# Optimization experiments

Measured on AMD Instinct MI355X. Metric: run time of the kernel, lower is better.

## Reference

```python
import jax, jax.numpy as jnp
import numpy as np

T, DIM, H = 1024, 2048, 16
QLR, KVLR = 1024, 512
NOPE, ROPE, VD = 128, 64, 128
QKD = NOPE + ROPE          # 192
IH, ID, TOPK = 16, 128, 256
EPS = 1e-6

def rmsnorm(x, w):
    return x * jax.lax.rsqrt(jnp.mean(x * x, axis=-1, keepdims=True) + EPS) * w

def layernorm(x, w, b, eps=1e-5):
    m = jnp.mean(x, axis=-1, keepdims=True)
    v = jnp.mean((x - m) ** 2, axis=-1, keepdims=True)
    return (x - m) * jax.lax.rsqrt(v + eps) * w + b

def apply_rope(x, cos, sin):
    # non-interleaved: first half = real, second half = imag
    d = x.shape[-1] // 2
    while cos.ndim < x.ndim:
        cos, sin = cos[:, None], sin[:, None]
    x1, x2 = x[..., :d], x[..., d:]
    return jnp.concatenate([x1 * cos - x2 * sin, x1 * sin + x2 * cos], axis=-1)

def hadamard(x):
    # unnormalized Walsh-Hadamard on last dim (power of 2)
    n = x.shape[-1]
    shape = x.shape
    y, h = x, 1
    while h < n:
        y = y.reshape(shape[:-1] + (-1, 2 * h))
        a, b = y[..., :h], y[..., h:]
        y = jnp.concatenate([a + b, a - b], axis=-1)
        h *= 2
    return y.reshape(shape)

def rotate_activation(x):
    # half-swap then Hadamard on each half
    d = x.shape[-1] // 2
    x1, x2 = x[..., :d], x[..., d:]
    return jnp.concatenate([hadamard(x2), hadamard(x1)], axis=-1)

def setup_inputs() -> dict:
    key = jax.random.key(0)
    ks = jax.random.split(key, 10)
    s = 0.02
    w = lambda k, shp: jax.random.normal(k, shp, jnp.float32) * s
    pos = jnp.arange(T, dtype=jnp.float32)
    inv = 1.0 / (10000.0 ** (jnp.arange(0, ROPE, 2, dtype=jnp.float32) / ROPE))
    ang = pos[:, None] * inv[None, :]
    return {
        'hidden_states': jax.random.normal(ks[0], (T, DIM), jnp.float32),
        'rope_cos': jnp.cos(ang), 'rope_sin': jnp.sin(ang),
        'wq_a': w(ks[1], (QLR, DIM)),
        'q_norm_w': jnp.ones((QLR,), jnp.float32),
        'wq_b': w(ks[2], (H * QKD, QLR)),
        'wkv_a': w(ks[3], (KVLR + ROPE, DIM)),
        'kv_norm_w': jnp.ones((KVLR,), jnp.float32),
        'wkv_b': w(ks[4], (H * (NOPE + VD), KVLR)),
        'wo': w(ks[5], (DIM, H * VD)),
        'iq_norm_w': jnp.ones((QLR,), jnp.float32),
        'iwq_b': w(ks[6], (IH * ID, QLR)),
        'iwk': w(ks[7], (IH * ID, DIM)),
        'k_norm_w': jnp.ones((ID,), jnp.float32),
        'k_norm_b': jnp.zeros((ID,), jnp.float32),
        'wproj': w(ks[8], (IH, DIM)),
    }

def reference(hidden_states, rope_cos, rope_sin, wq_a, q_norm_w, wq_b,
              wkv_a, kv_norm_w, wkv_b, wo, iq_norm_w, iwq_b, iwk,
              k_norm_w, k_norm_b, wproj):
    x = hidden_states
    t = x.shape[0]
    qr = x @ wq_a.T                                   # [t, QLR]

    # ---- lightning indexer: top-k causal token selection ----
    iq = (rmsnorm(qr, iq_norm_w) @ iwq_b.T).reshape(t, IH, ID)
    iq = jnp.concatenate([apply_rope(iq[..., :ROPE], rope_cos, rope_sin), iq[..., ROPE:]], -1)
    iq = rotate_activation(iq)
    ik = layernorm((x @ iwk.T).reshape(t, IH, ID), k_norm_w, k_norm_b)
    ik = jnp.concatenate([apply_rope(ik[..., :ROPE], rope_cos, rope_sin), ik[..., ROPE:]], -1)
    ik = rotate_activation(ik)
    w = (x @ wproj.T) * (IH ** -0.5) * (ID ** -0.5)   # [t, IH]
    dots = jax.nn.relu(jnp.einsum('thd,shd->ths', iq, ik)) * w[:, :, None]
    score = dots.sum(axis=1)                          # [t, t]
    rows = jnp.arange(t)
    score = jnp.where(rows[None, :] <= rows[:, None], score, -jnp.inf)
    _, topk_idx = jax.lax.top_k(score, TOPK)          # [t, TOPK]
    valid = topk_idx <= rows[:, None]
    safe_idx = jnp.where(valid, topk_idx, 0)

    # ---- MLA latent projections ----
    q = (rmsnorm(qr, q_norm_w) @ wq_b.T).reshape(t, H, QKD)
    q_nope, q_pe = q[..., :NOPE], q[..., NOPE:]
    q_pe = apply_rope(q_pe, rope_cos, rope_sin)
    kv_a = x @ wkv_a.T                                # [t, KVLR+ROPE]
    kv = rmsnorm(kv_a[:, :KVLR], kv_norm_w)
    k_pe = apply_rope(kv_a[:, KVLR:], rope_cos, rope_sin)
    wkv = wkv_b.reshape(H, NOPE + VD, KVLR)
    w_k, w_v = wkv[:, :NOPE, :], wkv[:, NOPE:, :]
    q_nope_proj = jnp.einsum('thd,hdc->thc', q_nope, w_k)
    q_key = jnp.concatenate([q_nope_proj, q_pe], -1)  # [t, H, KVLR+ROPE]
    kv_key = jnp.concatenate([kv, k_pe], -1)          # [t, KVLR+ROPE]

    # ---- sparse attention over selected indices ----
    sel = kv_key[safe_idx]                            # [t, TOPK, KVLR+ROPE]
    scale = QKD ** -0.5
    logits = jnp.einsum('thc,tkc->thk', q_key, sel) * scale
    logits = jnp.where(valid[:, None, :], logits, -jnp.inf)
    attn = jax.nn.softmax(logits, axis=-1)
    out_latent = jnp.einsum('thk,tkc->thc', attn, sel[..., :KVLR])
    out_v = jnp.einsum('thc,hdc->thd', out_latent, w_v)
    return out_v.reshape(t, H * VD) @ wo.T            # [t, DIM]
```

## Files before the change

kernel.cpp:

```cpp
#include <hip/hip_runtime.h>
#include <hip/hip_bf16.h>
#include <math.h>

#define T_     1024
#define DIM_   2048
#define H_     16
#define QLR_   1024
#define KVLR_  512
#define NOPE_  128
#define ROPE_  64
#define VD_    128
#define QKD_   192
#define IH_    16
#define ID_    128
#define TOPK_  256
#define CKV_   576

#define SCALE_W    0.022097086912079608f
#define SCALE_LOG  0.07216878364870323f

typedef short bfrag __attribute__((ext_vector_type(8)));
typedef float ffrag __attribute__((ext_vector_type(4)));

__device__ __forceinline__ unsigned short f2bf(float f) {
    union { __hip_bfloat16 h; unsigned short u; } c; c.h = __float2bfloat16(f); return c.u;
}
__device__ __forceinline__ float bf2f(unsigned short u) {
    union { unsigned short u; __hip_bfloat16 h; } c; c.u = u; return __bfloat162float(c.h);
}

__global__ __launch_bounds__(256) void cast_hl_k(
    const float* __restrict__ in, unsigned short* __restrict__ hi,
    unsigned short* __restrict__ lo, long n)
{
    long base = ((long)blockIdx.x * 256 + threadIdx.x) * 4;
    if (base >= n) return;
    float4 v = *(const float4*)(in + base);
    ushort4 h4;
    h4.x = f2bf(v.x); h4.y = f2bf(v.y); h4.z = f2bf(v.z); h4.w = f2bf(v.w);
    *(ushort4*)(hi + base) = h4;
    if (lo) {
        ushort4 l4;
        l4.x = f2bf(v.x - bf2f(h4.x));
        l4.y = f2bf(v.y - bf2f(h4.y));
        l4.z = f2bf(v.z - bf2f(h4.z));
        l4.w = f2bf(v.w - bf2f(h4.w));
        *(ushort4*)(lo + base) = l4;
    }
}

struct CastSeg { const float* src; unsigned short* hi; unsigned short* lo; };
struct CastDesc { CastSeg seg[6]; int bstart[7]; int nseg; };

__global__ __launch_bounds__(256) void castm_k(CastDesc d)
{
    int b = blockIdx.x, s = 0;
    #pragma unroll
    for (int i = 1; i < 6; ++i) if (i < d.nseg && b >= d.bstart[i]) s = i;
    long base = ((long)(b - d.bstart[s]) * 256 + threadIdx.x) * 4;
    float4 v = *(const float4*)(d.seg[s].src + base);
    ushort4 h4;
    h4.x = f2bf(v.x); h4.y = f2bf(v.y); h4.z = f2bf(v.z); h4.w = f2bf(v.w);
    *(ushort4*)(d.seg[s].hi + base) = h4;
    if (d.seg[s].lo) {
        ushort4 l4;
        l4.x = f2bf(v.x - bf2f(h4.x));
        l4.y = f2bf(v.y - bf2f(h4.y));
        l4.z = f2bf(v.z - bf2f(h4.z));
        l4.w = f2bf(v.w - bf2f(h4.w));
        *(ushort4*)(d.seg[s].lo + base) = l4;
    }
}

__global__ __launch_bounds__(256) void qrnorm_k(const float* __restrict__ qr,
    const float* __restrict__ iqw, const float* __restrict__ qw,
    unsigned short* __restrict__ qriq_hi, unsigned short* __restrict__ qriq_lo,
    unsigned short* __restrict__ qrq_hi)
{
    int t = blockIdx.x, tid = threadIdx.x;
    long base = (long)t * QLR_ + tid * 4;
    float4 v = *(const float4*)(qr + base);
    __shared__ float red[256];
    red[tid] = v.x * v.x + v.y * v.y + v.z * v.z + v.w * v.w;
    __syncthreads();
    for (int off = 128; off; off >>= 1) { if (tid < off) red[tid] += red[tid + off]; __syncthreads(); }
    float r = rsqrtf(red[0] / (float)QLR_ + 1e-6f);
    int col = tid * 4;
    float4 wi = *(const float4*)(iqw + col);
    float4 wq = *(const float4*)(qw + col);
    float s[4] = {v.x, v.y, v.z, v.w};
    float wiv[4] = {wi.x, wi.y, wi.z, wi.w};
    float wqv[4] = {wq.x, wq.y, wq.z, wq.w};
    ushort4 h4, l4, g4;
    unsigned short* hp = (unsigned short*)&h4;
    unsigned short* lp = (unsigned short*)&l4;
    unsigned short* gp = (unsigned short*)&g4;
    #pragma unroll
    for (int i = 0; i < 4; ++i) {
        float ai = s[i] * wiv[i] * r;
        float aq = s[i] * wqv[i] * r;
        hp[i] = f2bf(ai);
        lp[i] = f2bf(ai - bf2f(hp[i]));
        gp[i] = f2bf(aq);
    }
    *(ushort4*)(qriq_hi + base) = h4;
    *(ushort4*)(qriq_lo + base) = l4;
    *(ushort4*)(qrq_hi + base) = g4;
}

__global__ __launch_bounds__(256) void tcast_k(const float* __restrict__ in,
                                               unsigned short* __restrict__ out)
{
    int h = blockIdx.z, c0 = blockIdx.x * 32, d0 = blockIdx.y * 32;
    __shared__ float t[32][33];
    int tx = threadIdx.x & 31, ty = threadIdx.x >> 5;
    #pragma unroll
    for (int i = 0; i < 4; ++i)
        t[ty + i * 8][tx] = in[(long)(h * 256 + d0 + ty + i * 8) * 512 + c0 + tx];
    __syncthreads();
    #pragma unroll
    for (int i = 0; i < 4; ++i)
        out[((long)h * 512 + c0 + ty + i * 8) * 128 + d0 + tx] = f2bf(t[tx][ty + i * 8]);
}

__global__ __launch_bounds__(256) void gemm_bt_mfma_k(
    const unsigned short* __restrict__ A, const unsigned short* __restrict__ B,
    void* __restrict__ Cv, long sA, long sB, long sC,
    int lda, int ldb, int ldc, int N, int K, int obf)
{
    A += (long)blockIdx.z * sA;
    B += (long)blockIdx.z * sB;
    __shared__ unsigned short As[128 * 40];
    __shared__ unsigned short Bs[128 * 40];
    const int tid = threadIdx.x;
    const int bm = blockIdx.y * 128, bn = blockIdx.x * 128;
    const int wave = tid >> 6, lane = tid & 63;
    const int wm = (wave >> 1) * 64, wn = (wave & 1) * 64;
    const int lm = lane & 15, quad = lane >> 4;

    ffrag acc[4][4];
    #pragma unroll
    for (int mi = 0; mi < 4; ++mi)
        #pragma unroll
        for (int ni = 0; ni < 4; ++ni)
            #pragma unroll
            for (int r = 0; r < 4; ++r) acc[mi][ni][r] = 0.f;

    const int srow = tid >> 1, shalf = tid & 1;
    const long aoff = (long)(bm + srow) * lda + shalf * 16;
    int brow = bn + srow; if (brow > N - 1) brow = N - 1;
    const long boff = (long)brow * ldb + shalf * 16;
    unsigned short* la = As + srow * 40 + shalf * 16;
    unsigned short* lb = Bs + srow * 40 + shalf * 16;

    uint4 va0 = *(const uint4*)(A + aoff);
    uint4 va1 = *(const uint4*)(A + aoff + 8);
    uint4 vb0 = *(const uint4*)(B + boff);
    uint4 vb1 = *(const uint4*)(B + boff + 8);

    for (int k0 = 0; k0 < K; k0 += 32) {
        __syncthreads();
        *(uint4*)la = va0; *(uint4*)(la + 8) = va1;
        *(uint4*)lb = vb0; *(uint4*)(lb + 8) = vb1;
        __syncthreads();
        if (k0 + 32 < K) {
            va0 = *(const uint4*)(A + aoff + k0 + 32);
            va1 = *(const uint4*)(A + aoff + k0 + 40);
            vb0 = *(const uint4*)(B + boff + k0 + 32);
            vb1 = *(const uint4*)(B + boff + k0 + 40);
        }
        bfrag af[4], bf[4];
        #pragma unroll
        for (int mi = 0; mi < 4; ++mi)
            af[mi] = *(const bfrag*)(As + (wm + mi * 16 + lm) * 40 + quad * 8);
        #pragma unroll
        for (int ni = 0; ni < 4; ++ni)
            bf[ni] = *(const bfrag*)(Bs + (wn + ni * 16 + lm) * 40 + quad * 8);
        #pragma unroll
        for (int mi = 0; mi < 4; ++mi)
            #pragma unroll
            for (int ni = 0; ni < 4; ++ni)
                acc[mi][ni] = __builtin_amdgcn_mfma_f32_16x16x32_bf16(
                    af[mi], bf[ni], acc[mi][ni], 0, 0, 0);
    }

    #pragma unroll
    for (int mi = 0; mi < 4; ++mi)
        #pragma unroll
        for (int ni = 0; ni < 4; ++ni) {
            int n = bn + wn + ni * 16 + lm;
            if (n < N) {
                int mb = bm + wm + mi * 16 + quad * 4;
                if (obf) {
                    unsigned short* C = (unsigned short*)Cv + (long)blockIdx.z * sC;
                    #pragma unroll
                    for (int r = 0; r < 4; ++r)
                        C[(long)(mb + r) * ldc + n] = f2bf(acc[mi][ni][r]);
                } else {
                    float* C = (float*)Cv + (long)blockIdx.z * sC;
                    #pragma unroll
                    for (int r = 0; r < 4; ++r)
                        C[(long)(mb + r) * ldc + n] = acc[mi][ni][r];
                }
            }
        }
}

__global__ __launch_bounds__(256) void gemm_bt64_k(
    const unsigned short* __restrict__ A, const unsigned short* __restrict__ B,
    void* __restrict__ Cv, long sA, long sB, long sC,
    int lda, int ldb, int ldc, int N, int K, int obf)
{
    A += (long)blockIdx.z * sA;
    B += (long)blockIdx.z * sB;
    __shared__ unsigned short As[64 * 72];
    __shared__ unsigned short Bs[64 * 72];
    const int tid = threadIdx.x;
    const int bm = blockIdx.y * 64, bn = blockIdx.x * 64;
    const int wave = tid >> 6, lane = tid & 63;
    const int wm = (wave >> 1) * 32, wn = (wave & 1) * 32;
    const int lm = lane & 15, quad = lane >> 4;

    ffrag acc[2][2];
    #pragma unroll
    for (int mi = 0; mi < 2; ++mi)
        #pragma unroll
        for (int ni = 0; ni < 2; ++ni)
            #pragma unroll
            for (int r = 0; r < 4; ++r) acc[mi][ni][r] = 0.f;

    const int srow = tid >> 2, schunk = tid & 3;
    const long aoff = (long)(bm + srow) * lda + schunk * 8;
    int brow = bn + srow; if (brow > N - 1) brow = N - 1;
    const long boff = (long)brow * ldb + schunk * 8;
    const int loff = srow * 72 + schunk * 8;

    uint4 va0 = *(const uint4*)(A + aoff);
    uint4 va1 = *(const uint4*)(A + aoff + 32);
    uint4 vb0 = *(const uint4*)(B + boff);
    uint4 vb1 = *(const uint4*)(B + boff + 32);

    for (int k0 = 0; k0 < K; k0 += 64) {
        __syncthreads();
        *(uint4*)(As + loff) = va0; *(uint4*)(As + loff + 32) = va1;
        *(uint4*)(Bs + loff) = vb0; *(uint4*)(Bs + loff + 32) = vb1;
        __syncthreads();
        if (k0 + 64 < K) {
            va0 = *(const uint4*)(A + aoff + k0 + 64);
            va1 = *(const uint4*)(A + aoff + k0 + 96);
            vb0 = *(const uint4*)(B + boff + k0 + 64);
            vb1 = *(const uint4*)(B + boff + k0 + 96);
        }
        bfrag af[2][2], bf[2][2];
        #pragma unroll
        for (int mi = 0; mi < 2; ++mi)
            #pragma unroll
            for (int ks = 0; ks < 2; ++ks)
                af[mi][ks] = *(const bfrag*)(As + (wm + mi * 16 + lm) * 72 + ks * 32 + quad * 8);
        #pragma unroll
        for (int ni = 0; ni < 2; ++ni)
            #pragma unroll
            for (int ks = 0; ks < 2; ++ks)
                bf[ni][ks] = *(const bfrag*)(Bs + (wn + ni * 16 + lm) * 72 + ks * 32 + quad * 8);
        #pragma unroll
        for (int mi = 0; mi < 2; ++mi)
            #pragma unroll
            for (int ni = 0; ni < 2; ++ni) {
                acc[mi][ni] = __builtin_amdgcn_mfma_f32_16x16x32_bf16(af[mi][0], bf[ni][0], acc[mi][ni], 0, 0, 0);
                acc[mi][ni] = __builtin_amdgcn_mfma_f32_16x16x32_bf16(af[mi][1], bf[ni][1], acc[mi][ni], 0, 0, 0);
            }
    }

    #pragma unroll
    for (int mi = 0; mi < 2; ++mi)
        #pragma unroll
        for (int ni = 0; ni < 2; ++ni) {
            int n = bn + wn + ni * 16 + lm;
            if (n < N) {
                int mb = bm + wm + mi * 16 + quad * 4;
                if (obf) {
                    unsigned short* C = (unsigned short*)Cv + (long)blockIdx.z * sC;
                    #pragma unroll
                    for (int r = 0; r < 4; ++r)
                        C[(long)(mb + r) * ldc + n] = f2bf(acc[mi][ni][r]);
                } else {
                    float* C = (float*)Cv + (long)blockIdx.z * sC;
                    #pragma unroll
                    for (int r = 0; r < 4; ++r)
                        C[(long)(mb + r) * ldc + n] = acc[mi][ni][r];
                }
            }
        }
}

__global__ __launch_bounds__(256) void gemm3_bt64_k(
    const unsigned short* __restrict__ Ah, const unsigned short* __restrict__ Al,
    const unsigned short* __restrict__ Bh, const unsigned short* __restrict__ Bl,
    float* __restrict__ C, int lda, int ldb, int ldc, int K)
{
    __shared__ unsigned short Ahs[64 * 72], Als[64 * 72], Bhs[64 * 72], Bls[64 * 72];
    const int tid = threadIdx.x;
    const int bm = blockIdx.y * 64, bn = blockIdx.x * 64;
    const int wave = tid >> 6, lane = tid & 63;
    const int wm = (wave >> 1) * 32, wn = (wave & 1) * 32;
    const int lm = lane & 15, quad = lane >> 4;

    ffrag acc[2][2];
    #pragma unroll
    for (int mi = 0; mi < 2; ++mi)
        #pragma unroll
        for (int ni = 0; ni < 2; ++ni)
            #pragma unroll
            for (int r = 0; r < 4; ++r) acc[mi][ni][r] = 0.f;

    const int srow = tid >> 2, schunk = tid & 3;
    const long aoff = (long)(bm + srow) * lda + schunk * 8;
    const long boff = (long)(bn + srow) * ldb + schunk * 8;
    const int loff = srow * 72 + schunk * 8;

    uint4 vah0 = *(const uint4*)(Ah + aoff);
    uint4 vah1 = *(const uint4*)(Ah + aoff + 32);
    uint4 val0 = *(const uint4*)(Al + aoff);
    uint4 val1 = *(const uint4*)(Al + aoff + 32);
    uint4 vbh0 = *(const uint4*)(Bh + boff);
    uint4 vbh1 = *(const uint4*)(Bh + boff + 32);
    uint4 vbl0 = *(const uint4*)(Bl + boff);
    uint4 vbl1 = *(const uint4*)(Bl + boff + 32);

    for (int k0 = 0; k0 < K; k0 += 64) {
        __syncthreads();
        *(uint4*)(Ahs + loff) = vah0; *(uint4*)(Ahs + loff + 32) = vah1;
        *(uint4*)(Als + loff) = val0; *(uint4*)(Als + loff + 32) = val1;
        *(uint4*)(Bhs + loff) = vbh0; *(uint4*)(Bhs + loff + 32) = vbh1;
        *(uint4*)(Bls + loff) = vbl0; *(uint4*)(Bls + loff + 32) = vbl1;
        __syncthreads();
        if (k0 + 64 < K) {
            vah0 = *(const uint4*)(Ah + aoff + k0 + 64);
            vah1 = *(const uint4*)(Ah + aoff + k0 + 96);
            val0 = *(const uint4*)(Al + aoff + k0 + 64);
            val1 = *(const uint4*)(Al + aoff + k0 + 96);
            vbh0 = *(const uint4*)(Bh + boff + k0 + 64);
            vbh1 = *(const uint4*)(Bh + boff + k0 + 96);
            vbl0 = *(const uint4*)(Bl + boff + k0 + 64);
            vbl1 = *(const uint4*)(Bl + boff + k0 + 96);
        }
        bfrag ah[2][2], al[2][2], bh[2][2], bl[2][2];
        #pragma unroll
        for (int mi = 0; mi < 2; ++mi)
            #pragma unroll
            for (int ks = 0; ks < 2; ++ks) {
                ah[mi][ks] = *(const bfrag*)(Ahs + (wm + mi * 16 + lm) * 72 + ks * 32 + quad * 8);
                al[mi][ks] = *(const bfrag*)(Als + (wm + mi * 16 + lm) * 72 + ks * 32 + quad * 8);
            }
        #pragma unroll
        for (int ni = 0; ni < 2; ++ni)
            #pragma unroll
            for (int ks = 0; ks < 2; ++ks) {
                bh[ni][ks] = *(const bfrag*)(Bhs + (wn + ni * 16 + lm) * 72 + ks * 32 + quad * 8);
                bl[ni][ks] = *(const bfrag*)(Bls + (wn + ni * 16 + lm) * 72 + ks * 32 + quad * 8);
            }
        #pragma unroll
        for (int mi = 0; mi < 2; ++mi)
            #pragma unroll
            for (int ni = 0; ni < 2; ++ni) {
                acc[mi][ni] = __builtin_amdgcn_mfma_f32_16x16x32_bf16(ah[mi][0], bh[ni][0], acc[mi][ni], 0, 0, 0);
                acc[mi][ni] = __builtin_amdgcn_mfma_f32_16x16x32_bf16(ah[mi][0], bl[ni][0], acc[mi][ni], 0, 0, 0);
                acc[mi][ni] = __builtin_amdgcn_mfma_f32_16x16x32_bf16(al[mi][0], bh[ni][0], acc[mi][ni], 0, 0, 0);
                acc[mi][ni] = __builtin_amdgcn_mfma_f32_16x16x32_bf16(ah[mi][1], bh[ni][1], acc[mi][ni], 0, 0, 0);
                acc[mi][ni] = __builtin_amdgcn_mfma_f32_16x16x32_bf16(ah[mi][1], bl[ni][1], acc[mi][ni], 0, 0, 0);
                acc[mi][ni] = __builtin_amdgcn_mfma_f32_16x16x32_bf16(al[mi][1], bh[ni][1], acc[mi][ni], 0, 0, 0);
            }
    }

    #pragma unroll
    for (int mi = 0; mi < 2; ++mi)
        #pragma unroll
        for (int ni = 0; ni < 2; ++ni) {
            int n = bn + wn + ni * 16 + lm;
            int mb = bm + wm + mi * 16 + quad * 4;
            #pragma unroll
            for (int r = 0; r < 4; ++r)
                C[(long)(mb + r) * ldc + n] = acc[mi][ni][r];
        }
}

__global__ __launch_bounds__(256) void wtok_k(const float* __restrict__ x,
    const float* __restrict__ wproj, float* __restrict__ wtok)
{
    int t = blockIdx.x, tid = threadIdx.x;
    __shared__ float xs[DIM_];
    for (int c = tid; c < DIM_; c += 256) xs[c] = x[(long)t * DIM_ + c];
    __syncthreads();
    int wave = tid >> 6, lane = tid & 63;
    #pragma unroll
    for (int i = 0; i < 4; ++i) {
        int h = wave * 4 + i;
        float s = 0.f;
        for (int c = lane; c < DIM_; c += 64) s += xs[c] * wproj[(long)h * DIM_ + c];
        for (int off = 32; off; off >>= 1) s += __shfl_xor(s, off, 64);
        if (lane == 0) wtok[(long)t * IH_ + h] = s * SCALE_W;
    }
}

__global__ __launch_bounds__(256) void transform_iq2_k(const float* __restrict__ iq,
    unsigned short* __restrict__ hi, unsigned short* __restrict__ lo,
    const float* __restrict__ cosb, const float* __restrict__ sinb)
{
    int row = blockIdx.x * 4 + (threadIdx.x >> 6);
    int p = threadIdx.x & 63;
    int t = row >> 4;
    float a = iq[(long)row * 128 + p];
    float b = iq[(long)row * 128 + 64 + p];
    float c = cosb[t * 32 + (p & 31)], sn = sinb[t * 32 + (p & 31)];
    float asw = __shfl_xor(a, 32, 64);
    a = (p < 32) ? (a * c - asw * sn) : (asw * sn + a * c);
    #pragma unroll
    for (int h = 1; h < 64; h <<= 1) {
        float a2 = __shfl_xor(a, h, 64);
        float b2 = __shfl_xor(b, h, 64);
        a = (p & h) ? (a2 - a) : (a + a2);
        b = (p & h) ? (b2 - b) : (b + b2);
    }
    unsigned short hb = f2bf(b), ha = f2bf(a);
    hi[(long)row * 128 + p] = hb;
    hi[(long)row * 128 + 64 + p] = ha;
    lo[(long)row * 128 + p] = f2bf(b - bf2f(hb));
    lo[(long)row * 128 + 64 + p] = f2bf(a - bf2f(ha));
}

__global__ __launch_bounds__(256) void transform_ik2_k(const float* __restrict__ ik,
    unsigned short* __restrict__ hi, unsigned short* __restrict__ lo,
    const float* __restrict__ knw, const float* __restrict__ knb,
    const float* __restrict__ cosb, const float* __restrict__ sinb)
{
    int row = blockIdx.x * 4 + (threadIdx.x >> 6);
    int p = threadIdx.x & 63;
    int t = row >> 4;
    float a = ik[(long)row * 128 + p];
    float b = ik[(long)row * 128 + 64 + p];
    float s = a + b;
    #pragma unroll
    for (int o = 1; o < 64; o <<= 1) s += __shfl_xor(s, o, 64);
    float m = s * (1.f / 128.f);
    float da = a - m, db = b - m;
    float v = da * da + db * db;
    #pragma unroll
    for (int o = 1; o < 64; o <<= 1) v += __shfl_xor(v, o, 64);
    float r = rsqrtf(v * (1.f / 128.f) + 1e-5f);
    a = da * r * knw[p] + knb[p];
    b = db * r * knw[64 + p] + knb[64 + p];
    float c = cosb[t * 32 + (p & 31)], sn = sinb[t * 32 + (p & 31)];
    float asw = __shfl_xor(a, 32, 64);
    a = (p < 32) ? (a * c - asw * sn) : (asw * sn + a * c);
    #pragma unroll
    for (int h = 1; h < 64; h <<= 1) {
        float a2 = __shfl_xor(a, h, 64);
        float b2 = __shfl_xor(b, h, 64);
        a = (p & h) ? (a2 - a) : (a + a2);
        b = (p & h) ? (b2 - b) : (b + b2);
    }
    unsigned short hb = f2bf(b), ha = f2bf(a);
    hi[(long)row * 128 + p] = hb;
    hi[(long)row * 128 + 64 + p] = ha;
    lo[(long)row * 128 + p] = f2bf(b - bf2f(hb));
    lo[(long)row * 128 + 64 + p] = f2bf(a - bf2f(ha));
}

__global__ __launch_bounds__(256) void transform_kv2_k(const float* __restrict__ kva,
    unsigned short* __restrict__ kvb, const float* __restrict__ kvnw,
    const float* __restrict__ cosb, const float* __restrict__ sinb)
{
    int t = blockIdx.x, tid = threadIdx.x;
    const float* a = kva + (long)t * CKV_;
    unsigned short* o = kvb + (long)t * CKV_;
    float v0 = a[tid], v1 = a[tid + 256];
    __shared__ float red[256];
    __shared__ float rsh;
    red[tid] = v0 * v0 + v1 * v1; __syncthreads();
    for (int off = 128; off; off >>= 1) { if (tid < off) red[tid] += red[tid + off]; __syncthreads(); }
    if (tid == 0) rsh = rsqrtf(red[0] / (float)KVLR_ + 1e-6f);
    __syncthreads();
    float rs = rsh;
    o[tid]       = f2bf(v0 * rs * kvnw[tid]);
    o[tid + 256] = f2bf(v1 * rs * kvnw[tid + 256]);
    if (tid < 32) {
        float x1 = a[512 + tid], x2 = a[544 + tid];
        float c = cosb[t * 32 + tid], sn = sinb[t * 32 + tid];
        o[512 + tid] = f2bf(x1 * c - x2 * sn);
        o[544 + tid] = f2bf(x1 * sn + x2 * c);
    }
}

__global__ __launch_bounds__(64) void qpe_k(const float* __restrict__ q,
    unsigned short* __restrict__ qkeyb,
    const float* __restrict__ cosb, const float* __restrict__ sinb)
{
    int row = blockIdx.x * 2 + (threadIdx.x >> 5);
    int i = threadIdx.x & 31;
    int t = row / H_;
    const float* qp = q + (long)row * QKD_ + NOPE_;
    float x1 = qp[i], x2 = qp[i + 32];
    float c = cosb[t * 32 + i], sn = sinb[t * 32 + i];
    unsigned short* o = qkeyb + (long)row * CKV_ + 512;
    o[i]      = f2bf(x1 * c - x2 * sn);
    o[i + 32] = f2bf(x1 * sn + x2 * c);
}

__global__ __launch_bounds__(256) void score3_k(
    const unsigned short* __restrict__ iqh, const unsigned short* __restrict__ iql,
    const unsigned short* __restrict__ ikh, const unsigned short* __restrict__ ikl,
    const float* __restrict__ wtok, float* __restrict__ score)
{
    const int bt = blockIdx.y, bs = blockIdx.x;
    if (bs > bt) return;
    __shared__ unsigned short Ah[64 * 72], Al[64 * 72], Bh[64 * 72], Bl[64 * 72];
    __shared__ float wts[64][16];
    const int tid = threadIdx.x;
    const int wave = tid >> 6, lane = tid & 63;
    const int wm = (wave >> 1) * 32, wn = (wave & 1) * 32;
    const int lm = lane & 15, quad = lane >> 4;
    const int t0 = bt * 64, s0 = bs * 64;
    const int srow = tid >> 2, schunk = tid & 3;
    const int loff = srow * 72 + schunk * 8;

    for (int e = tid; e < 1024; e += 256)
        wts[e >> 4][e & 15] = wtok[(long)(t0 + (e >> 4)) * IH_ + (e & 15)];

    const long abase = (long)(t0 + srow) * 2048 + schunk * 8;
    const long bbase = (long)(s0 + srow) * 2048 + schunk * 8;

    uint4 pah0 = *(const uint4*)(iqh + abase);
    uint4 pah1 = *(const uint4*)(iqh + abase + 32);
    uint4 pal0 = *(const uint4*)(iql + abase);
    uint4 pal1 = *(const uint4*)(iql + abase + 32);
    uint4 pbh0 = *(const uint4*)(ikh + bbase);
    uint4 pbh1 = *(const uint4*)(ikh + bbase + 32);
    uint4 pbl0 = *(const uint4*)(ikl + bbase);
    uint4 pbl1 = *(const uint4*)(ikl + bbase + 32);

    float accf[2][2][4] = {};

    for (int h = 0; h < IH_; ++h) {
        ffrag acch[2][2];
        #pragma unroll
        for (int mi = 0; mi < 2; ++mi)
            #pragma unroll
            for (int ni = 0; ni < 2; ++ni)
                #pragma unroll
                for (int r = 0; r < 4; ++r) acch[mi][ni][r] = 0.f;

        #pragma unroll
        for (int k0 = 0; k0 < ID_; k0 += 64) {
            __syncthreads();
            *(uint4*)(Ah + loff) = pah0; *(uint4*)(Ah + loff + 32) = pah1;
            *(uint4*)(Al + loff) = pal0; *(uint4*)(Al + loff + 32) = pal1;
            *(uint4*)(Bh + loff) = pbh0; *(uint4*)(Bh + loff + 32) = pbh1;
            *(uint4*)(Bl + loff) = pbl0; *(uint4*)(Bl + loff + 32) = pbl1;
            __syncthreads();
            int step = h * 2 + (k0 >> 6) + 1;
            if (step < 32) {
                int off = (step >> 1) * 128 + (step & 1) * 64;
                pah0 = *(const uint4*)(iqh + abase + off);
                pah1 = *(const uint4*)(iqh + abase + off + 32);
                pal0 = *(const uint4*)(iql + abase + off);
                pal1 = *(const uint4*)(iql + abase + off + 32);
                pbh0 = *(const uint4*)(ikh + bbase + off);
                pbh1 = *(const uint4*)(ikh + bbase + off + 32);
                pbl0 = *(const uint4*)(ikl + bbase + off);
                pbl1 = *(const uint4*)(ikl + bbase + off + 32);
            }
            bfrag ahf[2][2], alf[2][2], bhf[2][2], blf[2][2];
            #pragma unroll
            for (int mi = 0; mi < 2; ++mi)
                #pragma unroll
                for (int ks = 0; ks < 2; ++ks) {
                    ahf[mi][ks] = *(const bfrag*)(Ah + (wm + mi * 16 + lm) * 72 + ks * 32 + quad * 8);
                    alf[mi][ks] = *(const bfrag*)(Al + (wm + mi * 16 + lm) * 72 + ks * 32 + quad * 8);
                }
            #pragma unroll
            for (int ni = 0; ni < 2; ++ni)
                #pragma unroll
                for (int ks = 0; ks < 2; ++ks) {
                    bhf[ni][ks] = *(const bfrag*)(Bh + (wn + ni * 16 + lm) * 72 + ks * 32 + quad * 8);
                    blf[ni][ks] = *(const bfrag*)(Bl + (wn + ni * 16 + lm) * 72 + ks * 32 + quad * 8);
                }
            #pragma unroll
            for (int mi = 0; mi < 2; ++mi)
                #pragma unroll
                for (int ni = 0; ni < 2; ++ni) {
                    acch[mi][ni] = __builtin_amdgcn_mfma_f32_16x16x32_bf16(ahf[mi][0], bhf[ni][0], acch[mi][ni], 0, 0, 0);
                    acch[mi][ni] = __builtin_amdgcn_mfma_f32_16x16x32_bf16(ahf[mi][0], blf[ni][0], acch[mi][ni], 0, 0, 0);
                    acch[mi][ni] = __builtin_amdgcn_mfma_f32_16x16x32_bf16(alf[mi][0], bhf[ni][0], acch[mi][ni], 0, 0, 0);
                    acch[mi][ni] = __builtin_amdgcn_mfma_f32_16x16x32_bf16(ahf[mi][1], bhf[ni][1], acch[mi][ni], 0, 0, 0);
                    acch[mi][ni] = __builtin_amdgcn_mfma_f32_16x16x32_bf16(ahf[mi][1], blf[ni][1], acch[mi][ni], 0, 0, 0);
                    acch[mi][ni] = __builtin_amdgcn_mfma_f32_16x16x32_bf16(alf[mi][1], bhf[ni][1], acch[mi][ni], 0, 0, 0);
                }
        }
        #pragma unroll
        for (int mi = 0; mi < 2; ++mi) {
            float wr[4];
            #pragma unroll
            for (int r = 0; r < 4; ++r) wr[r] = wts[wm + mi * 16 + quad * 4 + r][h];
            #pragma unroll
            for (int ni = 0; ni < 2; ++ni)
                #pragma unroll
                for (int r = 0; r < 4; ++r)
                    accf[mi][ni][r] += fmaxf(acch[mi][ni][r], 0.f) * wr[r];
        }
    }
    #pragma unroll
    for (int mi = 0; mi < 2; ++mi)
        #pragma unroll
        for (int ni = 0; ni < 2; ++ni) {
            int s = s0 + wn + ni * 16 + lm;
            int tb = t0 + wm + mi * 16 + quad * 4;
            #pragma unroll
            for (int r = 0; r < 4; ++r)
                score[(long)(tb + r) * T_ + s] = accf[mi][ni][r];
        }
}

__global__ __launch_bounds__(512) void topk_k(const float* __restrict__ score, int* __restrict__ topk)
{
    int t = blockIdx.x, tid = threadIdx.x;
    __shared__ float v[1024];
    __shared__ int ix[1024];
    for (int i = tid; i < 1024; i += 512) {
        v[i] = (i <= t) ? score[(long)t * T_ + i] : -INFINITY;
        ix[i] = i;
    }
    __syncthreads();
    for (int k = 2; k <= 1024; k <<= 1) {
        for (int j = k >> 1; j > 0; j >>= 1) {
            for (int i = tid; i < 1024; i += 512) {
                int l = i ^ j;
                if (l > i) {
                    bool up = ((i & k) == 0);
                    float vi = v[i], vl = v[l];
                    int xi = ix[i], xl = ix[l];
                    bool iBetter = (vi > vl) || (vi == vl && xi < xl);
                    bool doSwap = up ? !iBetter : iBetter;
                    if (doSwap) { v[i] = vl; v[l] = vi; ix[i] = xl; ix[l] = xi; }
                }
            }
            __syncthreads();
        }
    }
    if (tid < 256) topk[(long)t * TOPK_ + tid] = ix[tid];
}

__global__ __launch_bounds__(256, 4) void attn3_k(
    const unsigned short* __restrict__ qkeyb, const unsigned short* __restrict__ kvb,
    const int* __restrict__ topkp, unsigned short* __restrict__ olat)
{
    __shared__ __align__(16) unsigned short U[13568];
    __shared__ float red[16 * 17];
    __shared__ int kidx[256];
    unsigned short* Qbf = U;
    float*          Lg  = (float*)U;
    unsigned short* VT0 = U;
    unsigned short* VT1 = U + 4608;
    unsigned short* Pbf = U + 9344;

    const int t = blockIdx.x, tid = threadIdx.x;
    const int wave = tid >> 6, lane = tid & 63;
    const int lm = lane & 15, quad = lane >> 4;

    kidx[tid] = topkp[(long)t * TOPK_ + tid];
    const uint2* q2 = (const uint2*)(qkeyb + (long)t * (H_ * CKV_));
    #pragma unroll
    for (int rep = 0; rep < 9; ++rep) {
        int e = rep * 256 + tid;
        uint2 v = q2[e];
        int f = e * 4, h = f / CKV_, c = f - h * CKV_;
        *(uint2*)(Qbf + h * 584 + c) = v;
    }
    int myk0 = topkp[(long)t * TOPK_ + wave * 64 + 0 * 16 + lm];
    int myk1 = topkp[(long)t * TOPK_ + wave * 64 + 1 * 16 + lm];
    int myk2 = topkp[(long)t * TOPK_ + wave * 64 + 2 * 16 + lm];
    int myk3 = topkp[(long)t * TOPK_ + wave * 64 + 3 * 16 + lm];
    __syncthreads();

    ffrag acc[4];
    #pragma unroll
    for (int ni = 0; ni < 4; ++ni)
        #pragma unroll
        for (int r = 0; r < 4; ++r) acc[ni][r] = 0.f;

    const unsigned short* kb0 = kvb + (long)myk0 * CKV_ + quad * 8;
    const unsigned short* kb1 = kvb + (long)myk1 * CKV_ + quad * 8;
    const unsigned short* kb2 = kvb + (long)myk2 * CKV_ + quad * 8;
    const unsigned short* kb3 = kvb + (long)myk3 * CKV_ + quad * 8;

    bfrag ba[4], bb[4], bc[4];
    #define LDT(DST, C) { \
        DST[0] = *(const bfrag*)(kb0 + (C)); \
        DST[1] = *(const bfrag*)(kb1 + (C)); \
        DST[2] = *(const bfrag*)(kb2 + (C)); \
        DST[3] = *(const bfrag*)(kb3 + (C)); }
    #define PHA_STEP(I, BUF) { \
        bfrag af = *(const bfrag*)(Qbf + lm * 584 + (I) * 32 + quad * 8); \
        _Pragma("unroll") \
        for (int ni = 0; ni < 4; ++ni) \
            acc[ni] = __builtin_amdgcn_mfma_f32_16x16x32_bf16(af, BUF[ni], acc[ni], 0, 0, 0); \
        if ((I) < 15) LDT(BUF, (I) * 32 + 96) }

    LDT(ba, 0) LDT(bb, 32) LDT(bc, 64)
    PHA_STEP(0, ba)  PHA_STEP(1, bb)  PHA_STEP(2, bc)
    PHA_STEP(3, ba)  PHA_STEP(4, bb)  PHA_STEP(5, bc)
    PHA_STEP(6, ba)  PHA_STEP(7, bb)  PHA_STEP(8, bc)
    PHA_STEP(9, ba)  PHA_STEP(10, bb) PHA_STEP(11, bc)
    PHA_STEP(12, ba) PHA_STEP(13, bb) PHA_STEP(14, bc)
    PHA_STEP(15, ba) PHA_STEP(16, bb) PHA_STEP(17, bc)
    #undef PHA_STEP
    #undef LDT

    __syncthreads();
    #pragma unroll
    for (int ni = 0; ni < 4; ++ni)
        #pragma unroll
        for (int r = 0; r < 4; ++r)
            Lg[(quad * 4 + r) * 260 + wave * 64 + ni * 16 + lm] = acc[ni][r];
    __syncthreads();

    {
        int h = tid >> 4, j = tid & 15;
        float m = -INFINITY;
        #pragma unroll
        for (int kk = 0; kk < 16; ++kk) {
            int key = j * 16 + kk;
            if (kidx[key] <= t) m = fmaxf(m, Lg[h * 260 + key]);
        }
        red[h * 17 + j] = m;
        __syncthreads();
        float mh = -INFINITY;
        #pragma unroll
        for (int jj = 0; jj < 16; ++jj) mh = fmaxf(mh, red[h * 17 + jj]);
        __syncthreads();
        float s = 0.f;
        float pv[16];
        #pragma unroll
        for (int kk = 0; kk < 16; ++kk) {
            int key = j * 16 + kk;
            float e = (kidx[key] <= t) ? expf(Lg[h * 260 + key] * SCALE_LOG - mh * SCALE_LOG) : 0.f;
            pv[kk] = e; s += e;
        }
        red[h * 17 + j] = s;
        __syncthreads();
        float sh = 0.f;
        #pragma unroll
        for (int jj = 0; jj < 16; ++jj) sh += red[h * 17 + jj];
        float inv = 1.f / sh;
        #pragma unroll
        for (int kk = 0; kk < 16; ++kk)
            Pbf[h * 264 + j * 16 + kk] = f2bf(pv[kk] * inv);
    }

    const int kpair = tid & 15, cgrp = tid >> 4;
    ffrag acc2[2];
    #pragma unroll
    for (int ci = 0; ci < 2; ++ci)
        #pragma unroll
        for (int r = 0; r < 4; ++r) acc2[ci][r] = 0.f;

    uint4 ga0, gb0, ga1, gb1;
    #define PREFB(GA, GB, IT) { \
        int ka_ = kidx[((IT) & 7) * 32 + 2 * kpair]; \
        int kb_ = kidx[((IT) & 7) * 32 + 2 * kpair + 1]; \
        long co_ = (long)(((IT) >> 3) * 128 + cgrp * 8); \
        GA = *(const uint4*)(kvb + (long)ka_ * CKV_ + co_); \
        GB = *(const uint4*)(kvb + (long)kb_ * CKV_ + co_); }
    #define STOREB(GA, GB, BUF) { \
        const unsigned short* pa_ = (const unsigned short*)&GA; \
        const unsigned short* pb_ = (const unsigned short*)&GB; \
        _Pragma("unroll") \
        for (int i_ = 0; i_ < 8; ++i_) \
            *(unsigned int*)((BUF) + (cgrp * 8 + i_) * 36 + 2 * kpair) = \
                (unsigned int)pa_[i_] | ((unsigned int)pb_[i_] << 16); }
    #define MFMAB(BUF, IT) { \
        bfrag pa = *(const bfrag*)(Pbf + lm * 264 + ((IT) & 7) * 32 + quad * 8); \
        _Pragma("unroll") \
        for (int ci = 0; ci < 2; ++ci) { \
            int c = wave * 32 + ci * 16 + lm; \
            bfrag bv; \
            ((uint2*)&bv)[0] = *(const uint2*)((BUF) + c * 36 + quad * 8); \
            ((uint2*)&bv)[1] = *(const uint2*)((BUF) + c * 36 + quad * 8 + 4); \
            acc2[ci] = __builtin_amdgcn_mfma_f32_16x16x32_bf16(pa, bv, acc2[ci], 0, 0, 0); } }
    #define OLATST(IT) { \
        int p_ = (IT) >> 3; \
        _Pragma("unroll") \
        for (int ci = 0; ci < 2; ++ci) \
            _Pragma("unroll") \
            for (int r = 0; r < 4; ++r) \
                olat[((long)t * H_ + quad * 4 + r) * 512 + p_ * 128 + wave * 32 + ci * 16 + lm] \
                    = f2bf(acc2[ci][r]); \
        _Pragma("unroll") \
        for (int ci = 0; ci < 2; ++ci) \
            _Pragma("unroll") \
            for (int r = 0; r < 4; ++r) acc2[ci][r] = 0.f; }
    #define LGKBAR() { asm volatile("s_waitcnt lgkmcnt(0)" ::: "memory"); \
                       __builtin_amdgcn_s_barrier(); }

    PREFB(ga0, gb0, 0);
    PREFB(ga1, gb1, 1);
    LGKBAR();
    STOREB(ga0, gb0, VT0);
    LGKBAR();
    for (int it = 0; it < 32; it += 2) {
        STOREB(ga1, gb1, VT1);
        MFMAB(VT0, it);
        if (it + 2 < 32) PREFB(ga0, gb0, it + 2);
        LGKBAR();
        if (it + 2 < 32) STOREB(ga0, gb0, VT0);
        MFMAB(VT1, it + 1);
        if (it + 3 < 32) PREFB(ga1, gb1, it + 3);
        if (((it + 1) & 7) == 7) OLATST(it + 1);
        LGKBAR();
    }
    #undef PREFB
    #undef STOREB
    #undef MFMAB
    #undef OLATST
    #undef LGKBAR
}

extern "C" void kernel_launch(void* const* d_in, const int* in_sizes, int n_in,
                              void* d_out, int out_size, void* d_ws, size_t ws_size,
                              hipStream_t stream)
{
    const float* x          = (const float*)d_in[0];
    const float* cosb       = (const float*)d_in[1];
    const float* sinb       = (const float*)d_in[2];
    const float* wq_a       = (const float*)d_in[3];
    const float* q_norm_w   = (const float*)d_in[4];
    const float* wq_b       = (const float*)d_in[5];
    const float* wkv_a      = (const float*)d_in[6];
    const float* kv_norm_w  = (const float*)d_in[7];
    const float* wkv_b      = (const float*)d_in[8];
    const float* wo         = (const float*)d_in[9];
    const float* iq_norm_w  = (const float*)d_in[10];
    const float* iwq_b      = (const float*)d_in[11];
    const float* iwk        = (const float*)d_in[12];
    const float* k_norm_w   = (const float*)d_in[13];
    const float* k_norm_b   = (const float*)d_in[14];
    const float* wproj      = (const float*)d_in[15];
    float* out = (float*)d_out;

    float* ws    = (float*)d_ws;
    float* qr    = ws;
    float* wtok  = ws + 1049600;
    int*   topk  = (int*)(ws + 1655808);
    float* qkey  = ws + 1917952;
    float* outv  = ws + 11355136;
    float* U0    = ws + 13452288;
    float* iq    = U0;
    float* ik    = U0 + 2097152;
    float* kva   = U0 + 4194304;
    float* qbuf  = U0 + 4784128;
    float* score = U0 + 7929856;

    unsigned short* qkey_u = (unsigned short*)qkey;
    unsigned short* wqa_hi  = qkey_u;
    unsigned short* wqa_lo  = qkey_u + 2097152;
    unsigned short* iwk_hi  = qkey_u + 4194304;
    unsigned short* iwk_lo  = qkey_u + 8388608;
    unsigned short* iwqb_hi = qkey_u + 12582912;
    unsigned short* iwqb_lo = qkey_u + 14680064;
    unsigned short* qriq_hi = qkey_u + 16777216;
    unsigned short* qriq_lo = qkey_u + 17825792;
    unsigned short* iqbf_hi = qkey_u;
    unsigned short* iqbf_lo = qkey_u + 2097152;
    unsigned short* ikbf_hi = qkey_u + 4194304;
    unsigned short* ikbf_lo = qkey_u + 6291456;
    unsigned short* qkey_bf = qkey_u;
    unsigned short* wkvb_bf = qkey_u + 9437184;
    unsigned short* wo_bf   = qkey_u + 11534336;
    unsigned short* q_u     = (unsigned short*)qbuf;
    unsigned short* x_hi    = q_u;
    unsigned short* x_lo    = q_u + 2097152;
    unsigned short* wkva_hi = q_u + 4194304;
    unsigned short* outv_u  = (unsigned short*)outv;
    unsigned short* wqb_hi  = outv_u;
    unsigned short* qrq_hi  = outv_u + 3145728;
    unsigned short* outv_bf = outv_u;
    unsigned short* qbf     = (unsigned short*)iq;
    unsigned short* wkT     = (unsigned short*)ik;
    unsigned short* kvb     = (unsigned short*)qr;
    unsigned short* olat_bf = (unsigned short*)U0;

    {
        CastDesc d;
        d.seg[0] = { x,      x_hi,    x_lo    };
        d.seg[1] = { wq_a,   wqa_hi,  wqa_lo  };
        d.seg[2] = { iwk,    iwk_hi,  iwk_lo  };
        d.seg[3] = { iwq_b,  iwqb_hi, iwqb_lo };
        d.seg[4] = { wkv_a,  wkva_hi, nullptr };
        d.seg[5] = { wq_b,   wqb_hi,  nullptr };
        d.bstart[0] = 0;     d.bstart[1] = 2048;  d.bstart[2] = 4096;
        d.bstart[3] = 8192;  d.bstart[4] = 10240; d.bstart[5] = 11392;
        d.bstart[6] = 14464; d.nseg = 6;
        castm_k<<<14464, 256, 0, stream>>>(d);
    }

    gemm3_bt64_k<<<dim3(QLR_/64, T_/64), 256, 0, stream>>>(
        x_hi, x_lo, wqa_hi, wqa_lo, qr, DIM_, DIM_, QLR_, DIM_);

    qrnorm_k<<<T_, 256, 0, stream>>>(qr, iq_norm_w, q_norm_w, qriq_hi, qriq_lo, qrq_hi);

    gemm3_bt64_k<<<dim3(IH_*ID_/64, T_/64), 256, 0, stream>>>(
        qriq_hi, qriq_lo, iwqb_hi, iwqb_lo, iq, QLR_, QLR_, IH_*ID_, QLR_);
    gemm3_bt64_k<<<dim3(IH_*ID_/64, T_/64), 256, 0, stream>>>(
        x_hi, x_lo, iwk_hi, iwk_lo, ik, DIM_, DIM_, IH_*ID_, DIM_);

    gemm_bt64_k<<<dim3((CKV_+63)/64, T_/64, 1), 256, 0, stream>>>(
        x_hi, wkva_hi, kva, 0,0,0, DIM_, DIM_, CKV_, CKV_, DIM_, 0);

    gemm_bt64_k<<<dim3(H_*QKD_/64, T_/64, 1), 256, 0, stream>>>(
        qrq_hi, wqb_hi, qbuf, 0,0,0, QLR_, QLR_, H_*QKD_, H_*QKD_, QLR_, 0);

    wtok_k<<<T_, 256, 0, stream>>>(x, wproj, wtok);

    transform_iq2_k<<<T_*IH_/4, 256, 0, stream>>>(iq, iqbf_hi, iqbf_lo, cosb, sinb);
    transform_ik2_k<<<T_*IH_/4, 256, 0, stream>>>(ik, ikbf_hi, ikbf_lo, k_norm_w, k_norm_b, cosb, sinb);
    transform_kv2_k<<<T_, 256, 0, stream>>>(kva, kvb, kv_norm_w, cosb, sinb);

    score3_k<<<dim3(T_/64, T_/64), 256, 0, stream>>>(iqbf_hi, iqbf_lo, ikbf_hi, ikbf_lo, wtok, score);
    topk_k<<<T_, 512, 0, stream>>>(score, topk);

    cast_hl_k<<<3072, 256, 0, stream>>>(qbuf, qbf, nullptr, 3145728L);
    tcast_k<<<dim3(16, 4, 16), 256, 0, stream>>>(wkv_b, wkT);
    qpe_k<<<T_*H_/2, 64, 0, stream>>>(qbuf, qkey_bf, cosb, sinb);
    gemm_bt_mfma_k<<<dim3(KVLR_/128, T_/128, H_), 256, 0, stream>>>(
        qbf, wkT, qkey_bf, 192L, 65536L, 576L, H_*QKD_, ID_, H_*CKV_, KVLR_, ID_, 1);

    attn3_k<<<T_, 256, 0, stream>>>(qkey_bf, kvb, topk, olat_bf);

    {
        CastDesc d;
        d.seg[0] = { wkv_b, wkvb_bf, nullptr };
        d.seg[1] = { wo,    wo_bf,   nullptr };
        d.seg[2] = d.seg[0]; d.seg[3] = d.seg[0]; d.seg[4] = d.seg[0]; d.seg[5] = d.seg[0];
        d.bstart[0] = 0; d.bstart[1] = 2048; d.bstart[2] = 6144;
        d.bstart[3] = 6144; d.bstart[4] = 6144; d.bstart[5] = 6144; d.bstart[6] = 6144;
        d.nseg = 2;
        castm_k<<<6144, 256, 0, stream>>>(d);
    }

    gemm_bt64_k<<<dim3(VD_/64, T_/64, H_), 256, 0, stream>>>(
        olat_bf, wkvb_bf + (long)NOPE_*KVLR_, outv_bf,
        512L, (long)(NOPE_+VD_)*KVLR_, (long)VD_,
        H_*KVLR_, KVLR_, H_*VD_, VD_, KVLR_, 1);

    gemm_bt64_k<<<dim3(DIM_/64, T_/64, 1), 256, 0, stream>>>(
        outv_bf, wo_bf, out, 0,0,0, H_*VD_, H_*VD_, DIM_, DIM_, H_*VD_, 0);

    (void)in_sizes; (void)n_in; (void)out_size; (void)ws_size;
}
```

Baseline: 535.9 us.

## Merge independent GEMMs, casts and transforms into multi-segment kernel launches

Introduces a generic descriptor-driven kernel that dispatches each block to a GEMM (single or three-pass split bf16), a cast, a transpose-cast, the wtok projection or q rope, based on segment ranges. Independent work such as the q_a and index-k projections plus wtok, or the index-q GEMM with the kv_a GEMM and weight casts, now shares one launch. The per-row transforms are merged into one kernel as well. This cuts launch count and tail idle time, at the cost of a larger shared-memory footprint and more registers in the single-pass GEMM path, plus runtime mode branching.

```diff
diff --git a/kernel.cpp b/kernel.cpp
--- a/kernel.cpp
+++ b/kernel.cpp
@@ -27,26 +27,6 @@
 }
 __device__ __forceinline__ float bf2f(unsigned short u) {
     union { unsigned short u; __hip_bfloat16 h; } c; c.u = u; return __bfloat162float(c.h);
-}
-
-__global__ __launch_bounds__(256) void cast_hl_k(
-    const float* __restrict__ in, unsigned short* __restrict__ hi,
-    unsigned short* __restrict__ lo, long n)
-{
-    long base = ((long)blockIdx.x * 256 + threadIdx.x) * 4;
-    if (base >= n) return;
-    float4 v = *(const float4*)(in + base);
-    ushort4 h4;
-    h4.x = f2bf(v.x); h4.y = f2bf(v.y); h4.z = f2bf(v.z); h4.w = f2bf(v.w);
-    *(ushort4*)(hi + base) = h4;
-    if (lo) {
-        ushort4 l4;
-        l4.x = f2bf(v.x - bf2f(h4.x));
-        l4.y = f2bf(v.y - bf2f(h4.y));
-        l4.z = f2bf(v.z - bf2f(h4.z));
-        l4.w = f2bf(v.w - bf2f(h4.w));
-        *(ushort4*)(lo + base) = l4;
-    }
 }
 
 struct CastSeg { const float* src; unsigned short* hi; unsigned short* lo; };
@@ -108,21 +88,6 @@
     *(ushort4*)(qrq_hi + base) = g4;
 }
 
-__global__ __launch_bounds__(256) void tcast_k(const float* __restrict__ in,
-                                               unsigned short* __restrict__ out)
-{
-    int h = blockIdx.z, c0 = blockIdx.x * 32, d0 = blockIdx.y * 32;
-    __shared__ float t[32][33];
-    int tx = threadIdx.x & 31, ty = threadIdx.x >> 5;
-    #pragma unroll
-    for (int i = 0; i < 4; ++i)
-        t[ty + i * 8][tx] = in[(long)(h * 256 + d0 + ty + i * 8) * 512 + c0 + tx];
-    __syncthreads();
-    #pragma unroll
-    for (int i = 0; i < 4; ++i)
-        out[((long)h * 512 + c0 + ty + i * 8) * 128 + d0 + tx] = f2bf(t[tx][ty + i * 8]);
-}
-
 __global__ __launch_bounds__(256) void gemm_bt_mfma_k(
     const unsigned short* __restrict__ A, const unsigned short* __restrict__ B,
     void* __restrict__ Cv, long sA, long sB, long sC,
@@ -206,17 +171,106 @@
         }
 }
 
-__global__ __launch_bounds__(256) void gemm_bt64_k(
-    const unsigned short* __restrict__ A, const unsigned short* __restrict__ B,
-    void* __restrict__ Cv, long sA, long sB, long sC,
-    int lda, int ldb, int ldc, int N, int K, int obf)
+struct GSeg {
+    const void* A; const void* Al; const void* B; const void* Bl;
+    void* C; void* C2;
+    long sA, sB, sC;
+    int lda, ldb, ldc, N, K, bnx, bmx, mode, obf;
+};
+struct GDesc { GSeg seg[4]; int bstart[5]; int nseg; };
+
+__global__ __launch_bounds__(256) void mgemm_k(GDesc d)
 {
-    A += (long)blockIdx.z * sA;
-    B += (long)blockIdx.z * sB;
-    __shared__ unsigned short As[64 * 72];
-    __shared__ unsigned short Bs[64 * 72];
+    __shared__ unsigned short Ahs[64 * 72], Als[64 * 72], Bhs[64 * 72], Bls[64 * 72];
     const int tid = threadIdx.x;
-    const int bm = blockIdx.y * 64, bn = blockIdx.x * 64;
+    const int b = blockIdx.x;
+    int s = 0;
+    #pragma unroll
+    for (int i = 1; i < 4; ++i) if (i < d.nseg && b >= d.bstart[i]) s = i;
+    const int rel = b - d.bstart[s];
+    const int mode = d.seg[s].mode;
+
+    if (mode == 2) {
+        const float* src = (const float*)d.seg[s].A;
+        unsigned short* hi = (unsigned short*)d.seg[s].C;
+        unsigned short* lo = (unsigned short*)d.seg[s].C2;
+        long base = ((long)rel * 256 + tid) * 4;
+        float4 v = *(const float4*)(src + base);
+        ushort4 h4;
+        h4.x = f2bf(v.x); h4.y = f2bf(v.y); h4.z = f2bf(v.z); h4.w = f2bf(v.w);
+        *(ushort4*)(hi + base) = h4;
+        if (lo) {
+            ushort4 l4;
+            l4.x = f2bf(v.x - bf2f(h4.x));
+            l4.y = f2bf(v.y - bf2f(h4.y));
+            l4.z = f2bf(v.z - bf2f(h4.z));
+            l4.w = f2bf(v.w - bf2f(h4.w));
+            *(ushort4*)(lo + base) = l4;
+        }
+        return;
+    }
+    if (mode == 3) {
+        const float* x = (const float*)d.seg[s].A;
+        const float* wproj = (const float*)d.seg[s].B;
+        float* wt = (float*)d.seg[s].C;
+        float* xs = (float*)Ahs;
+        int t = rel;
+        for (int c = tid; c < DIM_; c += 256) xs[c] = x[(long)t * DIM_ + c];
+        __syncthreads();
+        int wave = tid >> 6, lane = tid & 63;
+        #pragma unroll
+        for (int i = 0; i < 4; ++i) {
+            int h = wave * 4 + i;
+            float sum = 0.f;
+            for (int c = lane; c < DIM_; c += 64) sum += xs[c] * wproj[(long)h * DIM_ + c];
+            for (int off = 32; off; off >>= 1) sum += __shfl_xor(sum, off, 64);
+            if (lane == 0) wt[(long)t * IH_ + h] = sum * SCALE_W;
+        }
+        return;
+    }
+    if (mode == 4) {
+        const float* in = (const float*)d.seg[s].A;
+        unsigned short* out = (unsigned short*)d.seg[s].C;
+        int h = rel >> 6, c0 = (rel & 15) * 32, d0 = ((rel >> 4) & 3) * 32;
+        float (*tt)[33] = (float(*)[33])(void*)Ahs;
+        int tx = tid & 31, ty = tid >> 5;
+        #pragma unroll
+        for (int i = 0; i < 4; ++i)
+            tt[ty + i * 8][tx] = in[(long)(h * 256 + d0 + ty + i * 8) * 512 + c0 + tx];
+        __syncthreads();
+        #pragma unroll
+        for (int i = 0; i < 4; ++i)
+            out[((long)h * 512 + c0 + ty + i * 8) * 128 + d0 + tx] = f2bf(tt[tx][ty + i * 8]);
+        return;
+    }
+    if (mode == 5) {
+        const float* q = (const float*)d.seg[s].A;
+        const float* cosb = (const float*)d.seg[s].B;
+        const float* sinb = (const float*)d.seg[s].Bl;
+        unsigned short* qk = (unsigned short*)d.seg[s].C;
+        int row = rel * 8 + (tid >> 5);
+        int i = tid & 31;
+        int t = row / H_;
+        const float* qp = q + (long)row * QKD_ + NOPE_;
+        float x1 = qp[i], x2 = qp[i + 32];
+        float c = cosb[t * 32 + i], sn = sinb[t * 32 + i];
+        unsigned short* o = qk + (long)row * CKV_ + 512;
+        o[i]      = f2bf(x1 * c - x2 * sn);
+        o[i + 32] = f2bf(x1 * sn + x2 * c);
+        return;
+    }
+
+    const GSeg g = d.seg[s];
+    const bool three = (mode == 1);
+    const int per = g.bnx * g.bmx;
+    const int z = rel / per;
+    const int r2 = rel - z * per;
+    const int bm = (r2 / g.bnx) * 64, bn = (r2 % g.bnx) * 64;
+    const unsigned short* A  = (const unsigned short*)g.A + (long)z * g.sA;
+    const unsigned short* B  = (const unsigned short*)g.B + (long)z * g.sB;
+    const unsigned short* Alp = (const unsigned short*)g.Al;
+    const unsigned short* Blp = (const unsigned short*)g.Bl;
+
     const int wave = tid >> 6, lane = tid & 63;
     const int wm = (wave >> 1) * 32, wn = (wave & 1) * 32;
     const int lm = lane & 15, quad = lane >> 4;
@@ -230,44 +284,81 @@
             for (int r = 0; r < 4; ++r) acc[mi][ni][r] = 0.f;
 
     const int srow = tid >> 2, schunk = tid & 3;
-    const long aoff = (long)(bm + srow) * lda + schunk * 8;
-    int brow = bn + srow; if (brow > N - 1) brow = N - 1;
-    const long boff = (long)brow * ldb + schunk * 8;
+    const long aoff = (long)(bm + srow) * g.lda + schunk * 8;
+    int brow = bn + srow; if (brow > g.N - 1) brow = g.N - 1;
+    const long boff = (long)brow * g.ldb + schunk * 8;
     const int loff = srow * 72 + schunk * 8;
 
-    uint4 va0 = *(const uint4*)(A + aoff);
-    uint4 va1 = *(const uint4*)(A + aoff + 32);
-    uint4 vb0 = *(const uint4*)(B + boff);
-    uint4 vb1 = *(const uint4*)(B + boff + 32);
-
-    for (int k0 = 0; k0 < K; k0 += 64) {
+    uint4 va0, va1, vb0, vb1, wa0, wa1, wb0, wb1;
+    va0 = *(const uint4*)(A + aoff);
+    va1 = *(const uint4*)(A + aoff + 32);
+    vb0 = *(const uint4*)(B + boff);
+    vb1 = *(const uint4*)(B + boff + 32);
+    if (three) {
+        wa0 = *(const uint4*)(Alp + aoff);
+        wa1 = *(const uint4*)(Alp + aoff + 32);
+        wb0 = *(const uint4*)(Blp + boff);
+        wb1 = *(const uint4*)(Blp + boff + 32);
+    }
+
+    for (int k0 = 0; k0 < g.K; k0 += 64) {
         __syncthreads();
-        *(uint4*)(As + loff) = va0; *(uint4*)(As + loff + 32) = va1;
-        *(uint4*)(Bs + loff) = vb0; *(uint4*)(Bs + loff + 32) = vb1;
+        *(uint4*)(Ahs + loff) = va0; *(uint4*)(Ahs + loff + 32) = va1;
+        *(uint4*)(Bhs + loff) = vb0; *(uint4*)(Bhs + loff + 32) = vb1;
+        if (three) {
+            *(uint4*)(Als + loff) = wa0; *(uint4*)(Als + loff + 32) = wa1;
+            *(uint4*)(Bls + loff) = wb0; *(uint4*)(Bls + loff + 32) = wb1;
+        }
         __syncthreads();
-        if (k0 + 64 < K) {
+        if (k0 + 64 < g.K) {
             va0 = *(const uint4*)(A + aoff + k0 + 64);
             va1 = *(const uint4*)(A + aoff + k0 + 96);
             vb0 = *(const uint4*)(B + boff + k0 + 64);
             vb1 = *(const uint4*)(B + boff + k0 + 96);
-        }
-        bfrag af[2][2], bf[2][2];
+            if (three) {
+                wa0 = *(const uint4*)(Alp + aoff + k0 + 64);
+                wa1 = *(const uint4*)(Alp + aoff + k0 + 96);
+                wb0 = *(const uint4*)(Blp + boff + k0 + 64);
+                wb1 = *(const uint4*)(Blp + boff + k0 + 96);
+            }
+        }
+        bfrag ah[2][2], bh[2][2], al[2][2], bl[2][2];
         #pragma unroll
         for (int mi = 0; mi < 2; ++mi)
             #pragma unroll
             for (int ks = 0; ks < 2; ++ks)
-                af[mi][ks] = *(const bfrag*)(As + (wm + mi * 16 + lm) * 72 + ks * 32 + quad * 8);
+                ah[mi][ks] = *(const bfrag*)(Ahs + (wm + mi * 16 + lm) * 72 + ks * 32 + quad * 8);
         #pragma unroll
         for (int ni = 0; ni < 2; ++ni)
             #pragma unroll
             for (int ks = 0; ks < 2; ++ks)
-                bf[ni][ks] = *(const bfrag*)(Bs + (wn + ni * 16 + lm) * 72 + ks * 32 + quad * 8);
+                bh[ni][ks] = *(const bfrag*)(Bhs + (wn + ni * 16 + lm) * 72 + ks * 32 + quad * 8);
+        if (three) {
+            #pragma unroll
+            for (int mi = 0; mi < 2; ++mi)
+                #pragma unroll
+                for (int ks = 0; ks < 2; ++ks)
+                    al[mi][ks] = *(const bfrag*)(Als + (wm + mi * 16 + lm) * 72 + ks * 32 + quad * 8);
+            #pragma unroll
+            for (int ni = 0; ni < 2; ++ni)
+                #pragma unroll
+                for (int ks = 0; ks < 2; ++ks)
+                    bl[ni][ks] = *(const bfrag*)(Bls + (wn + ni * 16 + lm) * 72 + ks * 32 + quad * 8);
+        }
         #pragma unroll
         for (int mi = 0; mi < 2; ++mi)
             #pragma unroll
             for (int ni = 0; ni < 2; ++ni) {
-                acc[mi][ni] = __builtin_amdgcn_mfma_f32_16x16x32_bf16(af[mi][0], bf[ni][0], acc[mi][ni], 0, 0, 0);
-                acc[mi][ni] = __builtin_amdgcn_mfma_f32_16x16x32_bf16(af[mi][1], bf[ni][1], acc[mi][ni], 0, 0, 0);
+                acc[mi][ni] = __builtin_amdgcn_mfma_f32_16x16x32_bf16(ah[mi][0], bh[ni][0], acc[mi][ni], 0, 0, 0);
+                if (three) {
+                    acc[mi][ni] = __builtin_amdgcn_mfma_f32_16x16x32_bf16(ah[mi][0], bl[ni][0], acc[mi][ni], 0, 0, 0);
+                    acc[mi][ni] = __builtin_amdgcn_mfma_f32_16x16x32_bf16(al[mi][0], bh[ni][0], acc[mi][ni], 0, 0, 0);
+                }
+                acc[mi][ni] = __builtin_amdgcn_mfma_f32_16x16x32_bf16(ah[mi][1], bh[ni][1], acc[mi][ni], 0, 0, 0);
+                if (three) {
+                    acc[mi][ni] = __builtin_amdgcn_mfma_f32_16x16x32_bf16(ah[mi][1], bl[ni][1], acc[mi][ni], 0, 0, 0);
+                    acc[mi][ni] = __builtin_amdgcn_mfma_f32_16x16x32_bf16(al[mi][1], bh[ni][1], acc[mi][ni], 0, 0, 0);
+                }
             }
     }
 
@@ -276,234 +367,91 @@
         #pragma unroll
         for (int ni = 0; ni < 2; ++ni) {
             int n = bn + wn + ni * 16 + lm;
-            if (n < N) {
+            if (n < g.N) {
                 int mb = bm + wm + mi * 16 + quad * 4;
-                if (obf) {
-                    unsigned short* C = (unsigned short*)Cv + (long)blockIdx.z * sC;
+                if (g.obf) {
+                    unsigned short* C = (unsigned short*)g.C + (long)z * g.sC;
                     #pragma unroll
                     for (int r = 0; r < 4; ++r)
-                        C[(long)(mb + r) * ldc + n] = f2bf(acc[mi][ni][r]);
+                        C[(long)(mb + r) * g.ldc + n] = f2bf(acc[mi][ni][r]);
                 } else {
-                    float* C = (float*)Cv + (long)blockIdx.z * sC;
+                    float* C = (float*)g.C + (long)z * g.sC;
                     #pragma unroll
                     for (int r = 0; r < 4; ++r)
-                        C[(long)(mb + r) * ldc + n] = acc[mi][ni][r];
+                        C[(long)(mb + r) * g.ldc + n] = acc[mi][ni][r];
                 }
             }
         }
 }
 
-__global__ __launch_bounds__(256) void gemm3_bt64_k(
-    const unsigned short* __restrict__ Ah, const unsigned short* __restrict__ Al,
-    const unsigned short* __restrict__ Bh, const unsigned short* __restrict__ Bl,
-    float* __restrict__ C, int lda, int ldb, int ldc, int K)
-{
-    __shared__ unsigned short Ahs[64 * 72], Als[64 * 72], Bhs[64 * 72], Bls[64 * 72];
-    const int tid = threadIdx.x;
-    const int bm = blockIdx.y * 64, bn = blockIdx.x * 64;
-    const int wave = tid >> 6, lane = tid & 63;
-    const int wm = (wave >> 1) * 32, wn = (wave & 1) * 32;
-    const int lm = lane & 15, quad = lane >> 4;
-
-    ffrag acc[2][2];
-    #pragma unroll
-    for (int mi = 0; mi < 2; ++mi)
-        #pragma unroll
-        for (int ni = 0; ni < 2; ++ni)
-            #pragma unroll
-            for (int r = 0; r < 4; ++r) acc[mi][ni][r] = 0.f;
-
-    const int srow = tid >> 2, schunk = tid & 3;
-    const long aoff = (long)(bm + srow) * lda + schunk * 8;
-    const long boff = (long)(bn + srow) * ldb + schunk * 8;
-    const int loff = srow * 72 + schunk * 8;
-
-    uint4 vah0 = *(const uint4*)(Ah + aoff);
-    uint4 vah1 = *(const uint4*)(Ah + aoff + 32);
-    uint4 val0 = *(const uint4*)(Al + aoff);
-    uint4 val1 = *(const uint4*)(Al + aoff + 32);
-    uint4 vbh0 = *(const uint4*)(Bh + boff);
-    uint4 vbh1 = *(const uint4*)(Bh + boff + 32);
-    uint4 vbl0 = *(const uint4*)(Bl + boff);
-    uint4 vbl1 = *(const uint4*)(Bl + boff + 32);
-
-    for (int k0 = 0; k0 < K; k0 += 64) {
-        __syncthreads();
-        *(uint4*)(Ahs + loff) = vah0; *(uint4*)(Ahs + loff + 32) = vah1;
-        *(uint4*)(Als + loff) = val0; *(uint4*)(Als + loff + 32) = val1;
-        *(uint4*)(Bhs + loff) = vbh0; *(uint4*)(Bhs + loff + 32) = vbh1;
-        *(uint4*)(Bls + loff) = vbl0; *(uint4*)(Bls + loff + 32) = vbl1;
-        __syncthreads();
-        if (k0 + 64 < K) {
-            vah0 = *(const uint4*)(Ah + aoff + k0 + 64);
-            vah1 = *(const uint4*)(Ah + aoff + k0 + 96);
-            val0 = *(const uint4*)(Al + aoff + k0 + 64);
-            val1 = *(const uint4*)(Al + aoff + k0 + 96);
-            vbh0 = *(const uint4*)(Bh + boff + k0 + 64);
-            vbh1 = *(const uint4*)(Bh + boff + k0 + 96);
-            vbl0 = *(const uint4*)(Bl + boff + k0 + 64);
-            vbl1 = *(const uint4*)(Bl + boff + k0 + 96);
-        }
-        bfrag ah[2][2], al[2][2], bh[2][2], bl[2][2];
-        #pragma unroll
-        for (int mi = 0; mi < 2; ++mi)
-            #pragma unroll
-            for (int ks = 0; ks < 2; ++ks) {
-                ah[mi][ks] = *(const bfrag*)(Ahs + (wm + mi * 16 + lm) * 72 + ks * 32 + quad * 8);
-                al[mi][ks] = *(const bfrag*)(Als + (wm + mi * 16 + lm) * 72 + ks * 32 + quad * 8);
-            }
-        #pragma unroll
-        for (int ni = 0; ni < 2; ++ni)
-            #pragma unroll
-            for (int ks = 0; ks < 2; ++ks) {
-                bh[ni][ks] = *(const bfrag*)(Bhs + (wn + ni * 16 + lm) * 72 + ks * 32 + quad * 8);
-                bl[ni][ks] = *(const bfrag*)(Bls + (wn + ni * 16 + lm) * 72 + ks * 32 + quad * 8);
-            }
-        #pragma unroll
-        for (int mi = 0; mi < 2; ++mi)
-            #pragma unroll
-            for (int ni = 0; ni < 2; ++ni) {
-                acc[mi][ni] = __builtin_amdgcn_mfma_f32_16x16x32_bf16(ah[mi][0], bh[ni][0], acc[mi][ni], 0, 0, 0);
-                acc[mi][ni] = __builtin_amdgcn_mfma_f32_16x16x32_bf16(ah[mi][0], bl[ni][0], acc[mi][ni], 0, 0, 0);
-                acc[mi][ni] = __builtin_amdgcn_mfma_f32_16x16x32_bf16(al[mi][0], bh[ni][0], acc[mi][ni], 0, 0, 0);
-                acc[mi][ni] = __builtin_amdgcn_mfma_f32_16x16x32_bf16(ah[mi][1], bh[ni][1], acc[mi][ni], 0, 0, 0);
-                acc[mi][ni] = __builtin_amdgcn_mfma_f32_16x16x32_bf16(ah[mi][1], bl[ni][1], acc[mi][ni], 0, 0, 0);
-                acc[mi][ni] = __builtin_amdgcn_mfma_f32_16x16x32_bf16(al[mi][1], bh[ni][1], acc[mi][ni], 0, 0, 0);
-            }
-    }
-
-    #pragma unroll
-    for (int mi = 0; mi < 2; ++mi)
-        #pragma unroll
-        for (int ni = 0; ni < 2; ++ni) {
-            int n = bn + wn + ni * 16 + lm;
-            int mb = bm + wm + mi * 16 + quad * 4;
-            #pragma unroll
-            for (int r = 0; r < 4; ++r)
-                C[(long)(mb + r) * ldc + n] = acc[mi][ni][r];
-        }
-}
-
-__global__ __launch_bounds__(256) void wtok_k(const float* __restrict__ x,
-    const float* __restrict__ wproj, float* __restrict__ wtok)
-{
-    int t = blockIdx.x, tid = threadIdx.x;
-    __shared__ float xs[DIM_];
-    for (int c = tid; c < DIM_; c += 256) xs[c] = x[(long)t * DIM_ + c];
-    __syncthreads();
-    int wave = tid >> 6, lane = tid & 63;
-    #pragma unroll
-    for (int i = 0; i < 4; ++i) {
-        int h = wave * 4 + i;
-        float s = 0.f;
-        for (int c = lane; c < DIM_; c += 64) s += xs[c] * wproj[(long)h * DIM_ + c];
-        for (int off = 32; off; off >>= 1) s += __shfl_xor(s, off, 64);
-        if (lane == 0) wtok[(long)t * IH_ + h] = s * SCALE_W;
-    }
-}
-
-__global__ __launch_bounds__(256) void transform_iq2_k(const float* __restrict__ iq,
-    unsigned short* __restrict__ hi, unsigned short* __restrict__ lo,
+__global__ __launch_bounds__(256) void mtrans_k(
+    const float* __restrict__ iq, unsigned short* __restrict__ iqh, unsigned short* __restrict__ iql,
+    const float* __restrict__ ik, unsigned short* __restrict__ ikh, unsigned short* __restrict__ ikl,
+    const float* __restrict__ knw, const float* __restrict__ knb,
+    const float* __restrict__ kva, unsigned short* __restrict__ kvb, const float* __restrict__ kvnw,
     const float* __restrict__ cosb, const float* __restrict__ sinb)
 {
-    int row = blockIdx.x * 4 + (threadIdx.x >> 6);
-    int p = threadIdx.x & 63;
-    int t = row >> 4;
-    float a = iq[(long)row * 128 + p];
-    float b = iq[(long)row * 128 + 64 + p];
-    float c = cosb[t * 32 + (p & 31)], sn = sinb[t * 32 + (p & 31)];
-    float asw = __shfl_xor(a, 32, 64);
-    a = (p < 32) ? (a * c - asw * sn) : (asw * sn + a * c);
-    #pragma unroll
-    for (int h = 1; h < 64; h <<= 1) {
-        float a2 = __shfl_xor(a, h, 64);
-        float b2 = __shfl_xor(b, h, 64);
-        a = (p & h) ? (a2 - a) : (a + a2);
-        b = (p & h) ? (b2 - b) : (b + b2);
-    }
-    unsigned short hb = f2bf(b), ha = f2bf(a);
-    hi[(long)row * 128 + p] = hb;
-    hi[(long)row * 128 + 64 + p] = ha;
-    lo[(long)row * 128 + p] = f2bf(b - bf2f(hb));
-    lo[(long)row * 128 + 64 + p] = f2bf(a - bf2f(ha));
-}
-
-__global__ __launch_bounds__(256) void transform_ik2_k(const float* __restrict__ ik,
-    unsigned short* __restrict__ hi, unsigned short* __restrict__ lo,
-    const float* __restrict__ knw, const float* __restrict__ knb,
-    const float* __restrict__ cosb, const float* __restrict__ sinb)
-{
-    int row = blockIdx.x * 4 + (threadIdx.x >> 6);
-    int p = threadIdx.x & 63;
-    int t = row >> 4;
-    float a = ik[(long)row * 128 + p];
-    float b = ik[(long)row * 128 + 64 + p];
-    float s = a + b;
-    #pragma unroll
-    for (int o = 1; o < 64; o <<= 1) s += __shfl_xor(s, o, 64);
-    float m = s * (1.f / 128.f);
-    float da = a - m, db = b - m;
-    float v = da * da + db * db;
-    #pragma unroll
-    for (int o = 1; o < 64; o <<= 1) v += __shfl_xor(v, o, 64);
-    float r = rsqrtf(v * (1.f / 128.f) + 1e-5f);
-    a = da * r * knw[p] + knb[p];
-    b = db * r * knw[64 + p] + knb[64 + p];
-    float c = cosb[t * 32 + (p & 31)], sn = sinb[t * 32 + (p & 31)];
-    float asw = __shfl_xor(a, 32, 64);
-    a = (p < 32) ? (a * c - asw * sn) : (asw * sn + a * c);
-    #pragma unroll
-    for (int h = 1; h < 64; h <<= 1) {
-        float a2 = __shfl_xor(a, h, 64);
-        float b2 = __shfl_xor(b, h, 64);
-        a = (p & h) ? (a2 - a) : (a + a2);
-        b = (p & h) ? (b2 - b) : (b + b2);
-    }
-    unsigned short hb = f2bf(b), ha = f2bf(a);
-    hi[(long)row * 128 + p] = hb;
-    hi[(long)row * 128 + 64 + p] = ha;
-    lo[(long)row * 128 + p] = f2bf(b - bf2f(hb));
-    lo[(long)row * 128 + 64 + p] = f2bf(a - bf2f(ha));
-}
-
-__global__ __launch_bounds__(256) void transform_kv2_k(const float* __restrict__ kva,
-    unsigned short* __restrict__ kvb, const float* __restrict__ kvnw,
-    const float* __restrict__ cosb, const float* __restrict__ sinb)
-{
-    int t = blockIdx.x, tid = threadIdx.x;
-    const float* a = kva + (long)t * CKV_;
-    unsigned short* o = kvb + (long)t * CKV_;
-    float v0 = a[tid], v1 = a[tid + 256];
     __shared__ float red[256];
     __shared__ float rsh;
-    red[tid] = v0 * v0 + v1 * v1; __syncthreads();
-    for (int off = 128; off; off >>= 1) { if (tid < off) red[tid] += red[tid + off]; __syncthreads(); }
-    if (tid == 0) rsh = rsqrtf(red[0] / (float)KVLR_ + 1e-6f);
-    __syncthreads();
-    float rs = rsh;
-    o[tid]       = f2bf(v0 * rs * kvnw[tid]);
-    o[tid + 256] = f2bf(v1 * rs * kvnw[tid + 256]);
-    if (tid < 32) {
-        float x1 = a[512 + tid], x2 = a[544 + tid];
-        float c = cosb[t * 32 + tid], sn = sinb[t * 32 + tid];
-        o[512 + tid] = f2bf(x1 * c - x2 * sn);
-        o[544 + tid] = f2bf(x1 * sn + x2 * c);
-    }
-}
-
-__global__ __launch_bounds__(64) void qpe_k(const float* __restrict__ q,
-    unsigned short* __restrict__ qkeyb,
-    const float* __restrict__ cosb, const float* __restrict__ sinb)
-{
-    int row = blockIdx.x * 2 + (threadIdx.x >> 5);
-    int i = threadIdx.x & 31;
-    int t = row / H_;
-    const float* qp = q + (long)row * QKD_ + NOPE_;
-    float x1 = qp[i], x2 = qp[i + 32];
-    float c = cosb[t * 32 + i], sn = sinb[t * 32 + i];
-    unsigned short* o = qkeyb + (long)row * CKV_ + 512;
-    o[i]      = f2bf(x1 * c - x2 * sn);
-    o[i + 32] = f2bf(x1 * sn + x2 * c);
+    const int b = blockIdx.x, tid = threadIdx.x;
+    if (b < 8192) {
+        const bool isq = b < 4096;
+        int rb = isq ? b : b - 4096;
+        int row = rb * 4 + (tid >> 6);
+        int p = tid & 63;
+        int t = row >> 4;
+        const float* src = isq ? iq : ik;
+        float a = src[(long)row * 128 + p];
+        float bb = src[(long)row * 128 + 64 + p];
+        if (!isq) {
+            float ssum = a + bb;
+            #pragma unroll
+            for (int o = 1; o < 64; o <<= 1) ssum += __shfl_xor(ssum, o, 64);
+            float m = ssum * (1.f / 128.f);
+            float da = a - m, db = bb - m;
+            float v = da * da + db * db;
+            #pragma unroll
+            for (int o = 1; o < 64; o <<= 1) v += __shfl_xor(v, o, 64);
+            float r = rsqrtf(v * (1.f / 128.f) + 1e-5f);
+            a = da * r * knw[p] + knb[p];
+            bb = db * r * knw[64 + p] + knb[64 + p];
+        }
+        float c = cosb[t * 32 + (p & 31)], sn = sinb[t * 32 + (p & 31)];
+        float asw = __shfl_xor(a, 32, 64);
+        a = (p < 32) ? (a * c - asw * sn) : (asw * sn + a * c);
+        #pragma unroll
+        for (int h = 1; h < 64; h <<= 1) {
+            float a2 = __shfl_xor(a, h, 64);
+            float b2 = __shfl_xor(bb, h, 64);
+            a = (p & h) ? (a2 - a) : (a + a2);
+            bb = (p & h) ? (b2 - bb) : (bb + b2);
+        }
+        unsigned short* hi = isq ? iqh : ikh;
+        unsigned short* lo = isq ? iql : ikl;
+        unsigned short hb = f2bf(bb), ha = f2bf(a);
+        hi[(long)row * 128 + p] = hb;
+        hi[(long)row * 128 + 64 + p] = ha;
+        lo[(long)row * 128 + p] = f2bf(bb - bf2f(hb));
+        lo[(long)row * 128 + 64 + p] = f2bf(a - bf2f(ha));
+    } else {
+        int t = b - 8192;
+        const float* a = kva + (long)t * CKV_;
+        unsigned short* o = kvb + (long)t * CKV_;
+        float v0 = a[tid], v1 = a[tid + 256];
+        red[tid] = v0 * v0 + v1 * v1; __syncthreads();
+        for (int off = 128; off; off >>= 1) { if (tid < off) red[tid] += red[tid + off]; __syncthreads(); }
+        if (tid == 0) rsh = rsqrtf(red[0] / (float)KVLR_ + 1e-6f);
+        __syncthreads();
+        float rs = rsh;
+        o[tid]       = f2bf(v0 * rs * kvnw[tid]);
+        o[tid + 256] = f2bf(v1 * rs * kvnw[tid + 256]);
+        if (tid < 32) {
+            float x1 = a[512 + tid], x2 = a[544 + tid];
+            float c = cosb[t * 32 + tid], sn = sinb[t * 32 + tid];
+            o[512 + tid] = f2bf(x1 * c - x2 * sn);
+            o[544 + tid] = f2bf(x1 * sn + x2 * c);
+        }
+    }
 }
 
 __global__ __launch_bounds__(256) void score3_k(
@@ -874,7 +822,7 @@
     unsigned short* ikbf_lo = qkey_u + 6291456;
     unsigned short* qkey_bf = qkey_u;
     unsigned short* wkvb_bf = qkey_u + 9437184;
-    unsigned short* wo_bf   = qkey_u + 11534336;
+    unsigned short* wo_bf   = qkey_u;
     unsigned short* q_u     = (unsigned short*)qbuf;
     unsigned short* x_hi    = q_u;
     unsigned short* x_lo    = q_u + 2097152;
@@ -902,57 +850,101 @@
         castm_k<<<14464, 256, 0, stream>>>(d);
     }
 
-    gemm3_bt64_k<<<dim3(QLR_/64, T_/64), 256, 0, stream>>>(
-        x_hi, x_lo, wqa_hi, wqa_lo, qr, DIM_, DIM_, QLR_, DIM_);
+    {
+        GDesc d{};
+        d.nseg = 3;
+        d.bstart[0] = 0; d.bstart[1] = 256; d.bstart[2] = 768; d.bstart[3] = 1792;
+        GSeg& s0 = d.seg[0];
+        s0.A = x_hi; s0.Al = x_lo; s0.B = wqa_hi; s0.Bl = wqa_lo; s0.C = qr;
+        s0.lda = DIM_; s0.ldb = DIM_; s0.ldc = QLR_; s0.N = QLR_; s0.K = DIM_;
+        s0.bnx = 16; s0.bmx = 16; s0.mode = 1; s0.obf = 0;
+        GSeg& s1 = d.seg[1];
+        s1.A = x_hi; s1.Al = x_lo; s1.B = iwk_hi; s1.Bl = iwk_lo; s1.C = ik;
+        s1.lda = DIM_; s1.ldb = DIM_; s1.ldc = IH_ * ID_; s1.N = IH_ * ID_; s1.K = DIM_;
+        s1.bnx = 32; s1.bmx = 16; s1.mode = 1; s1.obf = 0;
+        GSeg& s2 = d.seg[2];
+        s2.A = x; s2.B = wproj; s2.C = wtok; s2.mode = 3;
+        mgemm_k<<<1792, 256, 0, stream>>>(d);
+    }
 
     qrnorm_k<<<T_, 256, 0, stream>>>(qr, iq_norm_w, q_norm_w, qriq_hi, qriq_lo, qrq_hi);
 
-    gemm3_bt64_k<<<dim3(IH_*ID_/64, T_/64), 256, 0, stream>>>(
-        qriq_hi, qriq_lo, iwqb_hi, iwqb_lo, iq, QLR_, QLR_, IH_*ID_, QLR_);
-    gemm3_bt64_k<<<dim3(IH_*ID_/64, T_/64), 256, 0, stream>>>(
-        x_hi, x_lo, iwk_hi, iwk_lo, ik, DIM_, DIM_, IH_*ID_, DIM_);
-
-    gemm_bt64_k<<<dim3((CKV_+63)/64, T_/64, 1), 256, 0, stream>>>(
-        x_hi, wkva_hi, kva, 0,0,0, DIM_, DIM_, CKV_, CKV_, DIM_, 0);
-
-    gemm_bt64_k<<<dim3(H_*QKD_/64, T_/64, 1), 256, 0, stream>>>(
-        qrq_hi, wqb_hi, qbuf, 0,0,0, QLR_, QLR_, H_*QKD_, H_*QKD_, QLR_, 0);
-
-    wtok_k<<<T_, 256, 0, stream>>>(x, wproj, wtok);
-
-    transform_iq2_k<<<T_*IH_/4, 256, 0, stream>>>(iq, iqbf_hi, iqbf_lo, cosb, sinb);
-    transform_ik2_k<<<T_*IH_/4, 256, 0, stream>>>(ik, ikbf_hi, ikbf_lo, k_norm_w, k_norm_b, cosb, sinb);
-    transform_kv2_k<<<T_, 256, 0, stream>>>(kva, kvb, kv_norm_w, cosb, sinb);
+    {
+        GDesc d{};
+        d.nseg = 3;
+        d.bstart[0] = 0; d.bstart[1] = 512; d.bstart[2] = 656; d.bstart[3] = 2704;
+        GSeg& s0 = d.seg[0];
+        s0.A = qriq_hi; s0.Al = qriq_lo; s0.B = iwqb_hi; s0.Bl = iwqb_lo; s0.C = iq;
+        s0.lda = QLR_; s0.ldb = QLR_; s0.ldc = IH_ * ID_; s0.N = IH_ * ID_; s0.K = QLR_;
+        s0.bnx = 32; s0.bmx = 16; s0.mode = 1; s0.obf = 0;
+        GSeg& s1 = d.seg[1];
+        s1.A = x_hi; s1.B = wkva_hi; s1.C = kva;
+        s1.lda = DIM_; s1.ldb = DIM_; s1.ldc = CKV_; s1.N = CKV_; s1.K = DIM_;
+        s1.bnx = 9; s1.bmx = 16; s1.mode = 0; s1.obf = 0;
+        GSeg& s2 = d.seg[2];
+        s2.A = wkv_b; s2.C = wkvb_bf; s2.C2 = nullptr; s2.mode = 2;
+        mgemm_k<<<2704, 256, 0, stream>>>(d);
+    }
+
+    {
+        GDesc d{};
+        d.nseg = 1;
+        d.bstart[0] = 0; d.bstart[1] = 768;
+        GSeg& s0 = d.seg[0];
+        s0.A = qrq_hi; s0.B = wqb_hi; s0.C = qbuf;
+        s0.lda = QLR_; s0.ldb = QLR_; s0.ldc = H_ * QKD_; s0.N = H_ * QKD_; s0.K = QLR_;
+        s0.bnx = 48; s0.bmx = 16; s0.mode = 0; s0.obf = 0;
+        mgemm_k<<<768, 256, 0, stream>>>(d);
+    }
+
+    mtrans_k<<<9216, 256, 0, stream>>>(iq, iqbf_hi, iqbf_lo, ik, ikbf_hi, ikbf_lo,
+                                       k_norm_w, k_norm_b, kva, kvb, kv_norm_w, cosb, sinb);
 
     score3_k<<<dim3(T_/64, T_/64), 256, 0, stream>>>(iqbf_hi, iqbf_lo, ikbf_hi, ikbf_lo, wtok, score);
     topk_k<<<T_, 512, 0, stream>>>(score, topk);
 
-    cast_hl_k<<<3072, 256, 0, stream>>>(qbuf, qbf, nullptr, 3145728L);
-    tcast_k<<<dim3(16, 4, 16), 256, 0, stream>>>(wkv_b, wkT);
-    qpe_k<<<T_*H_/2, 64, 0, stream>>>(qbuf, qkey_bf, cosb, sinb);
+    {
+        GDesc d{};
+        d.nseg = 3;
+        d.bstart[0] = 0; d.bstart[1] = 3072; d.bstart[2] = 4096; d.bstart[3] = 6144;
+        GSeg& s0 = d.seg[0];
+        s0.A = qbuf; s0.C = qbf; s0.C2 = nullptr; s0.mode = 2;
+        GSeg& s1 = d.seg[1];
+        s1.A = wkv_b; s1.C = wkT; s1.mode = 4;
+        GSeg& s2 = d.seg[2];
+        s2.A = qbuf; s2.B = cosb; s2.Bl = sinb; s2.C = qkey_bf; s2.mode = 5;
+        mgemm_k<<<6144, 256, 0, stream>>>(d);
+    }
+
     gemm_bt_mfma_k<<<dim3(KVLR_/128, T_/128, H_), 256, 0, stream>>>(
         qbf, wkT, qkey_bf, 192L, 65536L, 576L, H_*QKD_, ID_, H_*CKV_, KVLR_, ID_, 1);
 
     attn3_k<<<T_, 256, 0, stream>>>(qkey_bf, kvb, topk, olat_bf);
 
     {
-        CastDesc d;
-        d.seg[0] = { wkv_b, wkvb_bf, nullptr };
-        d.seg[1] = { wo,    wo_bf,   nullptr };
-        d.seg[2] = d.seg[0]; d.seg[3] = d.seg[0]; d.seg[4] = d.seg[0]; d.seg[5] = d.seg[0];
-        d.bstart[0] = 0; d.bstart[1] = 2048; d.bstart[2] = 6144;
-        d.bstart[3] = 6144; d.bstart[4] = 6144; d.bstart[5] = 6144; d.bstart[6] = 6144;
+        GDesc d{};
         d.nseg = 2;
-        castm_k<<<6144, 256, 0, stream>>>(d);
-    }
-
-    gemm_bt64_k<<<dim3(VD_/64, T_/64, H_), 256, 0, stream>>>(
-        olat_bf, wkvb_bf + (long)NOPE_*KVLR_, outv_bf,
-        512L, (long)(NOPE_+VD_)*KVLR_, (long)VD_,
-        H_*KVLR_, KVLR_, H_*VD_, VD_, KVLR_, 1);
-
-    gemm_bt64_k<<<dim3(DIM_/64, T_/64, 1), 256, 0, stream>>>(
-        outv_bf, wo_bf, out, 0,0,0, H_*VD_, H_*VD_, DIM_, DIM_, H_*VD_, 0);
+        d.bstart[0] = 0; d.bstart[1] = 512; d.bstart[2] = 4608;
+        GSeg& s0 = d.seg[0];
+        s0.A = olat_bf; s0.B = wkvb_bf + (long)NOPE_ * KVLR_; s0.C = outv_bf;
+        s0.sA = 512; s0.sB = (long)(NOPE_ + VD_) * KVLR_; s0.sC = VD_;
+        s0.lda = H_ * KVLR_; s0.ldb = KVLR_; s0.ldc = H_ * VD_; s0.N = VD_; s0.K = KVLR_;
+        s0.bnx = 2; s0.bmx = 16; s0.mode = 0; s0.obf = 1;
+        GSeg& s1 = d.seg[1];
+        s1.A = wo; s1.C = wo_bf; s1.C2 = nullptr; s1.mode = 2;
+        mgemm_k<<<4608, 256, 0, stream>>>(d);
+    }
+
+    {
+        GDesc d{};
+        d.nseg = 1;
+        d.bstart[0] = 0; d.bstart[1] = 512;
+        GSeg& s0 = d.seg[0];
+        s0.A = outv_bf; s0.B = wo_bf; s0.C = out;
+        s0.lda = H_ * VD_; s0.ldb = H_ * VD_; s0.ldc = DIM_; s0.N = DIM_; s0.K = H_ * VD_;
+        s0.bnx = 32; s0.bmx = 16; s0.mode = 0; s0.obf = 0;
+        mgemm_k<<<512, 256, 0, stream>>>(d);
+    }
 
     (void)in_sizes; (void)n_in; (void)out_size; (void)ws_size;
 }
```

Result: faster. 494.3 us (-7.8%).
